# Kernel tuning notes

Hardware: AMD Instinct MI355X
Metric: run time of the kernel (lower is better)

Reference implementation:

```python
import jax, jax.numpy as jnp
import numpy as np

N_SENT = 20  # sentence_number


def setup_inputs() -> dict:
    key = jax.random.key(0)
    k1, k2, k3, k4, k5 = jax.random.split(key, 5)
    B, S, D, U = 2048, 800, 100, 50
    inputs = jax.random.normal(k1, (B, S + 1, D), dtype=jnp.float32)
    # keras 'random_normal' initializer default stddev = 0.05
    vw = 0.05 * jax.random.normal(k2, (U, 1), dtype=jnp.float32)
    wh = 0.05 * jax.random.normal(k3, (U, D), dtype=jnp.float32)
    wu = 0.05 * jax.random.normal(k4, (U, D), dtype=jnp.float32)
    bw = 0.05 * jax.random.normal(k5, (U, 1), dtype=jnp.float32)
    return {"inputs": inputs, "vw": vw, "wh": wh, "wu": wu, "bw": bw}


def reference(inputs, vw, wh, wu, bw):
    # inputs: [B, S+1, D]; last row of each item is the user vector
    sent = inputs[:, :-1, :]          # [B, S, D]
    uvec = inputs[:, -1, :]           # [B, D]
    B, S, D = sent.shape
    sec = S // N_SENT
    h = sent.reshape(B, N_SENT, sec, D)               # sections of sentences
    # wu @ user_vec + bw  -> per-batch additive bias  [B, units]
    wub = uvec @ wu.T + bw[:, 0]
    # tanh(h @ wh.T + wub)                              [B, n, s, units]
    t = jnp.tanh(jnp.einsum('bnsd,ud->bnsu', h, wh) + wub[:, None, None, :])
    e = jnp.einsum('bnsu,u->bns', t, vw[:, 0])          # attention logits
    alpha = jax.nn.softmax(e, axis=-1)                  # softmax over section
    out = jnp.einsum('bns,bnsd->bnd', alpha, h)         # weighted pooling
    return out  # [B, N_SENT, D]
```

## Files before the change

### kernel.cpp

```cpp
#include <hip/hip_runtime.h>
#include <hip/hip_bf16.h>
#include <stdint.h>

#define NB    2048
#define NSENT 20
#define SEC   40
#define DD    100
#define UU    50
#define SP1   801
#define STRIDE 136

typedef short bf16x8 __attribute__((ext_vector_type(8)));
typedef float f32x4 __attribute__((ext_vector_type(4)));

__device__ __forceinline__ unsigned f2bf(float f) {
  unsigned u = __float_as_uint(f);
  return (u + 0x7fffu + ((u >> 16) & 1u)) >> 16;
}

__global__ __launch_bounds__(256, 5) void doc_kernel(
    const float* __restrict__ inputs, const float* __restrict__ vw,
    const float* __restrict__ wh, const float* __restrict__ wu,
    const float* __restrict__ bw, float* __restrict__ out) {
  __shared__ __align__(16) unsigned short hs[2][48 * STRIDE];
  __shared__ __align__(16) float epart[3 * 16 * 4];

  const int tid  = threadIdx.x;
  const int w    = tid >> 6, lane = tid & 63;
  const int col  = lane & 15, grp = lane >> 4;
  const int b    = blockIdx.x;

  const float4* base4 = (const float4*)(inputs + (size_t)b * SP1 * DD);

  float4 stage[4];
  #pragma unroll
  for (int j = 0; j < 4; ++j) {
    int idx = j * 256 + tid;
    if (idx < 1000) stage[j] = base4[idx];
  }

  {
    uint4 z; z.x = z.y = z.z = z.w = 0u;
    uint4* p = (uint4*)&hs[0][0];
    #pragma unroll 1
    for (int i = tid; i < 2 * 48 * STRIDE / 8; i += 256) p[i] = z;
  }

  int cvta[4];
  #pragma unroll
  for (int j = 0; j < 4; ++j) {
    int idx = j * 256 + tid;
    int row = idx / 25, c4 = idx - row * 25;
    cvta[j] = row * 272 + c4 * 8;
  }

  bf16x8 afrag[4];
  {
    int u = w * 16 + col;
    #pragma unroll
    for (int kt = 0; kt < 4; ++kt) {
      bf16x8 f;
      #pragma unroll
      for (int j = 0; j < 8; ++j) {
        int k = kt * 32 + grp * 8 + j;
        float v = (u < UU && k < DD) ? wh[u * DD + k] : 0.f;
        f[j] = (short)f2bf(v);
      }
      afrag[kt] = f;
    }
  }

  float wubacc;
  {
    int ur = lane < UU ? lane : UU - 1;
    const float4* uv4 = (const float4*)(inputs + ((size_t)b * SP1 + SP1 - 1) * DD);
    const float4* wr4 = (const float4*)(wu + ur * DD);
    float a0 = bw[ur];
    #pragma unroll 5
    for (int q = 0; q < 25; ++q) {
      float4 uq = uv4[q], wq = wr4[q];
      a0 = fmaf(uq.x, wq.x, a0); a0 = fmaf(uq.y, wq.y, a0);
      a0 = fmaf(uq.z, wq.z, a0); a0 = fmaf(uq.w, wq.w, a0);
    }
    wubacc = a0;
  }
  float vwr[4], wubr[4];
  #pragma unroll
  for (int r = 0; r < 4; ++r) {
    int u = w * 16 + grp * 4 + r;
    float wv = __shfl(wubacc, u & 63);
    bool val = (u < UU);
    vwr[r]  = val ? vw[u] : 0.f;
    wubr[r] = val ? wv : 0.f;
  }

  __syncthreads();

  float* outb = out + (size_t)b * NSENT * DD;

  #pragma unroll 1
  for (int t = 0; t < NSENT; ++t) {
    unsigned char* hc = (unsigned char*)&hs[t & 1][0];

    #pragma unroll
    for (int j = 0; j < 4; ++j) {
      int idx = j * 256 + tid;
      if (idx < 1000) {
        unsigned o0, o1;
        asm("v_cvt_pk_bf16_f32 %0, %1, %2" : "=v"(o0) : "v"(stage[j].x), "v"(stage[j].y));
        asm("v_cvt_pk_bf16_f32 %0, %1, %2" : "=v"(o1) : "v"(stage[j].z), "v"(stage[j].w));
        uint2 wv; wv.x = o0; wv.y = o1;
        *(uint2*)(hc + cvta[j]) = wv;
      }
    }
    __syncthreads();

    if (t + 1 < NSENT) {
      const float4* nb4 = base4 + (size_t)(t + 1) * 1000;
      #pragma unroll
      for (int j = 0; j < 4; ++j) {
        int idx = j * 256 + tid;
        if (idx < 1000) stage[j] = nb4[idx];
      }
    }
    __builtin_amdgcn_sched_barrier(0);

    f32x4 acc[3];
    #pragma unroll
    for (int st = 0; st < 3; ++st) { f32x4 z = {0.f,0.f,0.f,0.f}; acc[st] = z; }
    #pragma unroll
    for (int kt = 0; kt < 4; ++kt) {
      #pragma unroll
      for (int st = 0; st < 3; ++st) {
        bf16x8 hf = *(const bf16x8*)(hc + (st * 16 + col) * 272 + kt * 64 + grp * 16);
        acc[st] = __builtin_amdgcn_mfma_f32_16x16x32_bf16(afrag[kt], hf, acc[st], 0, 0, 0);
      }
    }

    #pragma unroll
    for (int st = 0; st < 3; ++st) {
      float s = 0.f;
      #pragma unroll
      for (int r = 0; r < 4; ++r) {
        float x = acc[st][r] + wubr[r];
        float E = __expf(2.f * x);
        float tt = 1.f - 2.f * __builtin_amdgcn_rcpf(E + 1.f);
        s = fmaf(tt, vwr[r], s);
      }
      s += __shfl_xor(s, 16);
      s += __shfl_xor(s, 32);
      if (grp == 0) epart[st * 64 + col * 4 + w] = s;
    }
    __syncthreads();

    int sl = lane < SEC ? lane : 0;
    f32x4 q = *(const f32x4*)&epart[(sl >> 4) * 64 + (sl & 15) * 4];
    float e = (q[0] + q[1]) + (q[2] + q[3]);
    float p = (lane < SEC) ? __expf(e) : 0.f;
    float sum = p;
    sum += __shfl_xor(sum, 1);
    sum += __shfl_xor(sum, 2);
    sum += __shfl_xor(sum, 4);
    sum += __shfl_xor(sum, 8);
    sum += __shfl_xor(sum, 16);
    sum += __shfl_xor(sum, 32);
    float pr = p * __builtin_amdgcn_rcpf(sum);
    asm volatile("" : "+v"(pr));

    if (lane < 25) {
      int d = 25 * w + lane;
      const unsigned short* hp = (const unsigned short*)hc + d;
      float a0 = 0.f, a1 = 0.f;
      #pragma unroll
      for (int s = 0; s < SEC; s += 2) {
        float al0 = __uint_as_float(__builtin_amdgcn_readlane(__float_as_uint(pr), s));
        float al1 = __uint_as_float(__builtin_amdgcn_readlane(__float_as_uint(pr), s + 1));
        a0 = fmaf(al0, __uint_as_float((unsigned)hp[s * STRIDE] << 16), a0);
        a1 = fmaf(al1, __uint_as_float((unsigned)hp[(s + 1) * STRIDE] << 16), a1);
      }
      outb[t * DD + d] = a0 + a1;
    }
  }
}

extern "C" void kernel_launch(void* const* d_in, const int* in_sizes, int n_in,
                              void* d_out, int out_size, void* d_ws, size_t ws_size,
                              hipStream_t stream) {
  const float* inputs = (const float*)d_in[0];
  const float* vw     = (const float*)d_in[1];
  const float* wh     = (const float*)d_in[2];
  const float* wu     = (const float*)d_in[3];
  const float* bw     = (const float*)d_in[4];
  float* out = (float*)d_out;

  doc_kernel<<<NB, 256, 0, stream>>>(inputs, vw, wh, wu, bw, out);
}
```

Measured before the change: 171.8 us.

## Prefetch two tiles ahead with dual register stages and relax occupancy bound

Global loads of each 40-row section now go into two alternating register staging sets, so the load for tile t+2 is issued while tile t is processed. The main loop is unrolled by two through a macro. The idx<1000 guards are dropped: the extra lanes read past the tile and write into the zero-padding rows 40-47 of the LDS tile, which the softmax never uses. Launch bounds drop from 5 to 4 waves per SIMD to make room for the extra staging registers. The goal is more global memory loads in flight to hide HBM latency, at the cost of lower occupancy.

After: 162.0 us. 5.7% less time.

```diff
diff --git a/kernel.cpp b/kernel.cpp
--- a/kernel.cpp
+++ b/kernel.cpp
@@ -18,7 +18,7 @@
   return (u + 0x7fffu + ((u >> 16) & 1u)) >> 16;
 }
 
-__global__ __launch_bounds__(256, 5) void doc_kernel(
+__global__ __launch_bounds__(256, 4) void doc_kernel(
     const float* __restrict__ inputs, const float* __restrict__ vw,
     const float* __restrict__ wh, const float* __restrict__ wu,
     const float* __restrict__ bw, float* __restrict__ out) {
@@ -32,12 +32,11 @@
 
   const float4* base4 = (const float4*)(inputs + (size_t)b * SP1 * DD);
 
-  float4 stage[4];
+  float4 stA[4], stB[4];
   #pragma unroll
-  for (int j = 0; j < 4; ++j) {
-    int idx = j * 256 + tid;
-    if (idx < 1000) stage[j] = base4[idx];
-  }
+  for (int j = 0; j < 4; ++j) stA[j] = base4[j * 256 + tid];
+  #pragma unroll
+  for (int j = 0; j < 4; ++j) stB[j] = base4[1000 + j * 256 + tid];
 
   {
     uint4 z; z.x = z.y = z.z = z.w = 0u;
@@ -98,89 +97,91 @@
 
   float* outb = out + (size_t)b * NSENT * DD;
 
+#define TILE_BODY(stg, t)                                                      \
+  {                                                                            \
+    unsigned char* hc = (unsigned char*)&hs[(t) & 1][0];                       \
+                     \
+    _Pragma("unroll")                                                          \
+    for (int j = 0; j < 4; ++j) {                                              \
+      unsigned o0, o1;                                                         \
+      asm("v_cvt_pk_bf16_f32 %0, %1, %2" : "=v"(o0) : "v"(stg[j].x), "v"(stg[j].y)); \
+      asm("v_cvt_pk_bf16_f32 %0, %1, %2" : "=v"(o1) : "v"(stg[j].z), "v"(stg[j].w)); \
+      uint2 wv; wv.x = o0; wv.y = o1;                                          \
+      *(uint2*)(hc + cvta[j]) = wv;                                            \
+    }                                                                          \
+      \
+    if ((t) + 2 < NSENT) {                                                     \
+      const float4* nb4 = base4 + (size_t)((t) + 2) * 1000;                    \
+      _Pragma("unroll")                                                        \
+      for (int j = 0; j < 4; ++j) stg[j] = nb4[j * 256 + tid];                 \
+    }                                                                          \
+    __builtin_amdgcn_sched_barrier(0);                                         \
+    __syncthreads();                                                   \
+                                   \
+    f32x4 acc[3];                                                              \
+    _Pragma("unroll")                                                          \
+    for (int st = 0; st < 3; ++st) { f32x4 z = {0.f,0.f,0.f,0.f}; acc[st] = z; } \
+    _Pragma("unroll")                                                          \
+    for (int kt = 0; kt < 4; ++kt) {                                           \
+      _Pragma("unroll")                                                        \
+      for (int st = 0; st < 3; ++st) {                                         \
+        bf16x8 hf = *(const bf16x8*)(hc + (st * 16 + col) * 272 + kt * 64 + grp * 16); \
+        acc[st] = __builtin_amdgcn_mfma_f32_16x16x32_bf16(afrag[kt], hf, acc[st], 0, 0, 0); \
+      }                                                                        \
+    }                                                                          \
+                                \
+    _Pragma("unroll")                                                          \
+    for (int st = 0; st < 3; ++st) {                                           \
+      float s = 0.f;                                                           \
+      _Pragma("unroll")                                                        \
+      for (int r = 0; r < 4; ++r) {                                            \
+        float x = acc[st][r] + wubr[r];                                        \
+        float E = __expf(2.f * x);                                             \
+        float tt = 1.f - 2.f * __builtin_amdgcn_rcpf(E + 1.f);                 \
+        s = fmaf(tt, vwr[r], s);                                               \
+      }                                                                        \
+      s += __shfl_xor(s, 16);                                                  \
+      s += __shfl_xor(s, 32);                                                  \
+      if (grp == 0) epart[st * 64 + col * 4 + w] = s;                          \
+    }                                                                          \
+    __syncthreads();                                                   \
+             \
+    int sl = lane < SEC ? lane : 0;                                            \
+    f32x4 q = *(const f32x4*)&epart[(sl >> 4) * 64 + (sl & 15) * 4];           \
+    float e = (q[0] + q[1]) + (q[2] + q[3]);                                   \
+    float p = (lane < SEC) ? __expf(e) : 0.f;                                  \
+    float sum = p;                                                             \
+    sum += __shfl_xor(sum, 1);                                                 \
+    sum += __shfl_xor(sum, 2);                                                 \
+    sum += __shfl_xor(sum, 4);                                                 \
+    sum += __shfl_xor(sum, 8);                                                 \
+    sum += __shfl_xor(sum, 16);                                                \
+    sum += __shfl_xor(sum, 32);                                                \
+    float pr = p * __builtin_amdgcn_rcpf(sum);                                 \
+        \
+    asm volatile("" : "+v"(pr));                                               \
+                  \
+    if (lane < 25) {                                                           \
+      int d = 25 * w + lane;                                                   \
+      const unsigned short* hp = (const unsigned short*)hc + d;                \
+      float a0 = 0.f, a1 = 0.f;                                                \
+      _Pragma("unroll")                                                        \
+      for (int s = 0; s < SEC; s += 2) {                                       \
+        float al0 = __uint_as_float(__builtin_amdgcn_readlane(__float_as_uint(pr), s));     \
+        float al1 = __uint_as_float(__builtin_amdgcn_readlane(__float_as_uint(pr), s + 1)); \
+        a0 = fmaf(al0, __uint_as_float((unsigned)hp[s * STRIDE] << 16), a0);   \
+        a1 = fmaf(al1, __uint_as_float((unsigned)hp[(s + 1) * STRIDE] << 16), a1); \
+      }                                                                        \
+      outb[(t) * DD + d] = a0 + a1;                                            \
+    }                                                                          \
+  }
+
   #pragma unroll 1
-  for (int t = 0; t < NSENT; ++t) {
-    unsigned char* hc = (unsigned char*)&hs[t & 1][0];
-
-    #pragma unroll
-    for (int j = 0; j < 4; ++j) {
-      int idx = j * 256 + tid;
-      if (idx < 1000) {
-        unsigned o0, o1;
-        asm("v_cvt_pk_bf16_f32 %0, %1, %2" : "=v"(o0) : "v"(stage[j].x), "v"(stage[j].y));
-        asm("v_cvt_pk_bf16_f32 %0, %1, %2" : "=v"(o1) : "v"(stage[j].z), "v"(stage[j].w));
-        uint2 wv; wv.x = o0; wv.y = o1;
-        *(uint2*)(hc + cvta[j]) = wv;
-      }
-    }
-    __syncthreads();
-
-    if (t + 1 < NSENT) {
-      const float4* nb4 = base4 + (size_t)(t + 1) * 1000;
-      #pragma unroll
-      for (int j = 0; j < 4; ++j) {
-        int idx = j * 256 + tid;
-        if (idx < 1000) stage[j] = nb4[idx];
-      }
-    }
-    __builtin_amdgcn_sched_barrier(0);
-
-    f32x4 acc[3];
-    #pragma unroll
-    for (int st = 0; st < 3; ++st) { f32x4 z = {0.f,0.f,0.f,0.f}; acc[st] = z; }
-    #pragma unroll
-    for (int kt = 0; kt < 4; ++kt) {
-      #pragma unroll
-      for (int st = 0; st < 3; ++st) {
-        bf16x8 hf = *(const bf16x8*)(hc + (st * 16 + col) * 272 + kt * 64 + grp * 16);
-        acc[st] = __builtin_amdgcn_mfma_f32_16x16x32_bf16(afrag[kt], hf, acc[st], 0, 0, 0);
-      }
-    }
-
-    #pragma unroll
-    for (int st = 0; st < 3; ++st) {
-      float s = 0.f;
-      #pragma unroll
-      for (int r = 0; r < 4; ++r) {
-        float x = acc[st][r] + wubr[r];
-        float E = __expf(2.f * x);
-        float tt = 1.f - 2.f * __builtin_amdgcn_rcpf(E + 1.f);
-        s = fmaf(tt, vwr[r], s);
-      }
-      s += __shfl_xor(s, 16);
-      s += __shfl_xor(s, 32);
-      if (grp == 0) epart[st * 64 + col * 4 + w] = s;
-    }
-    __syncthreads();
-
-    int sl = lane < SEC ? lane : 0;
-    f32x4 q = *(const f32x4*)&epart[(sl >> 4) * 64 + (sl & 15) * 4];
-    float e = (q[0] + q[1]) + (q[2] + q[3]);
-    float p = (lane < SEC) ? __expf(e) : 0.f;
-    float sum = p;
-    sum += __shfl_xor(sum, 1);
-    sum += __shfl_xor(sum, 2);
-    sum += __shfl_xor(sum, 4);
-    sum += __shfl_xor(sum, 8);
-    sum += __shfl_xor(sum, 16);
-    sum += __shfl_xor(sum, 32);
-    float pr = p * __builtin_amdgcn_rcpf(sum);
-    asm volatile("" : "+v"(pr));
-
-    if (lane < 25) {
-      int d = 25 * w + lane;
-      const unsigned short* hp = (const unsigned short*)hc + d;
-      float a0 = 0.f, a1 = 0.f;
-      #pragma unroll
-      for (int s = 0; s < SEC; s += 2) {
-        float al0 = __uint_as_float(__builtin_amdgcn_readlane(__float_as_uint(pr), s));
-        float al1 = __uint_as_float(__builtin_amdgcn_readlane(__float_as_uint(pr), s + 1));
-        a0 = fmaf(al0, __uint_as_float((unsigned)hp[s * STRIDE] << 16), a0);
-        a1 = fmaf(al1, __uint_as_float((unsigned)hp[(s + 1) * STRIDE] << 16), a1);
-      }
-      outb[t * DD + d] = a0 + a1;
-    }
+  for (int t = 0; t < NSENT; t += 2) {
+    TILE_BODY(stA, t)
+    TILE_BODY(stB, t + 1)
   }
+#undef TILE_BODY
 }
 
 extern "C" void kernel_launch(void* const* d_in, const int* in_sizes, int n_in,
```
